# Kernel tuning notes

Measured on AMD Instinct MI355X. Metric: run time of the kernel, lower is better.

Reference implementation:

```python
import jax, jax.numpy as jnp
import numpy as np

N = 50000       # nodes
E = 800000      # edges (avg degree 16)
IN_F = 128
OUT_F = 128
NEG_SLOPE = 0.2  # LeakyReLU alpha
EPS = 1e-10


def setup_inputs() -> dict:
    key = jax.random.key(0)
    k1, k2, k3, k4 = jax.random.split(key, 4)
    h = jax.random.normal(k1, (N, IN_F), dtype=jnp.float32)
    edge_index = jax.random.randint(k2, (2, E), 0, N, dtype=jnp.int32)
    # nn.Linear(in, out, bias=False): weight is [out, in], Wh = h @ W.T
    W = jax.random.normal(k3, (OUT_F, IN_F), dtype=jnp.float32) * (1.0 / np.sqrt(IN_F))
    # a: [2*out, 1], xavier_uniform with gain=1.414
    lim = 1.414 * np.sqrt(6.0 / (2 * OUT_F + 1))
    a = jax.random.uniform(k4, (2 * OUT_F, 1), dtype=jnp.float32, minval=-lim, maxval=lim)
    return {"h": h, "edge_index": edge_index, "W": W, "a": a}


def reference(h, edge_index, W, a):
    Wh = h @ W.T                              # [N, out]
    rows = edge_index[0]
    cols = edge_index[1]
    # cat([Wh_i, Wh_j],1) @ a  ==  (Wh @ a1)[rows] + (Wh @ a2)[cols]
    a1 = a[:OUT_F, 0]
    a2 = a[OUT_F:, 0]
    s1 = Wh @ a1                              # [N]
    s2 = Wh @ a2                              # [N]
    e = jax.nn.leaky_relu(s1[rows] + s2[cols], negative_slope=NEG_SLOPE)  # [E]
    e = e - jnp.max(e)
    exp_e = jnp.exp(e)
    sum_exp = jax.ops.segment_sum(exp_e, rows, num_segments=N)            # [N]
    alpha = exp_e / (sum_exp[rows] + EPS)                                 # [E]
    # sparse.mm(adj_att, Wh): h_prime[i] = sum_j alpha_ij * Wh[j]
    h_prime = jax.ops.segment_sum(alpha[:, None] * Wh[cols], rows, num_segments=N)
    return jax.nn.elu(h_prime)
```

## Files before the change

### kernel.cpp

```cpp
#include <hip/hip_runtime.h>

constexpr int FD = 128;
constexpr int NBMAX = 512;
constexpr int CH1 = 4096;
constexpr int CAPB = 3072;

typedef __attribute__((ext_vector_type(8))) short short8;
typedef __attribute__((ext_vector_type(4))) float floatx4;

__device__ __forceinline__ unsigned fenc(float f) {
    unsigned u = __float_as_uint(f);
    return (u & 0x80000000u) ? ~u : (u | 0x80000000u);
}
__device__ __forceinline__ float fdec(unsigned e) {
    return (e & 0x80000000u) ? __uint_as_float(e & 0x7fffffffu)
                             : __uint_as_float(~e);
}

__device__ __forceinline__ unsigned bpack(float x, float y) {
    unsigned ux = __float_as_uint(x); ux += 0x7FFFu + ((ux >> 16) & 1u);
    unsigned uy = __float_as_uint(y); uy += 0x7FFFu + ((uy >> 16) & 1u);
    return (ux >> 16) | (uy & 0xFFFF0000u);
}

__global__ __launch_bounds__(128) void initwt_kernel(const float* __restrict__ W,
                                                     unsigned* __restrict__ Wb,
                                                     int* __restrict__ bcursor,
                                                     unsigned* __restrict__ maxslot) {
    int j = blockIdx.x, k = threadIdx.x;
    float w = W[(size_t)j * FD + k];
    float pw = __shfl_xor(w, 1, 64);
    if ((k & 1) == 0) Wb[(size_t)j * 64 + (k >> 1)] = bpack(w, pw);
    if (j == 0) {
        for (int i = k; i < NBMAX; i += 128) bcursor[i] = 0;
        if (k < 2) maxslot[k] = 0x007FFFFFu;
    }
}

union GBShared {
    struct {
        int cnt[NBMAX];
        int ex[NBMAX];
        int gbase[NBMAX];
        int wtot[8];
        unsigned stage[CH1];
    } bin;
    struct {
        float m1[8];
        float m2[8];
    } gm;
};

__global__ __launch_bounds__(512) void gembin_kernel(const float* __restrict__ h,
                                                     const unsigned* __restrict__ Wb,
                                                     const float* __restrict__ a,
                                                     const int* __restrict__ ei,
                                                     int* __restrict__ bcursor,
                                                     unsigned* __restrict__ Whb,
                                                     float* __restrict__ s1,
                                                     float* __restrict__ s2,
                                                     unsigned* __restrict__ ebuf,
                                                     unsigned* __restrict__ maxslot,
                                                     int n, int e_cnt, int ngemm) {
    __shared__ GBShared sh;
    int t = threadIdx.x;

    if ((int)blockIdx.x < ngemm) {
        int w = t >> 6, lane = t & 63;
        int quad = lane >> 4, c = lane & 15;
        int rbase = blockIdx.x * 128 + w * 16;
        int node = rbase + c;

        int arow = min(node, n - 1);
        const floatx4* hrow = (const floatx4*)(h + (size_t)arow * FD);
        union { uint4 u; short8 s; } hf[4];
#pragma unroll
        for (int kk = 0; kk < 4; ++kk) {
            int k0 = kk * 32 + quad * 8;
            floatx4 f0 = __builtin_nontemporal_load(hrow + (k0 >> 2));
            floatx4 f1 = __builtin_nontemporal_load(hrow + (k0 >> 2) + 1);
            hf[kk].u.x = bpack(f0.x, f0.y);
            hf[kk].u.y = bpack(f0.z, f0.w);
            hf[kk].u.z = bpack(f1.x, f1.y);
            hf[kk].u.w = bpack(f1.z, f1.w);
        }

        float p1 = 0.f, p2 = 0.f;

#pragma unroll
        for (int tt = 0; tt < 8; ++tt) {
            const uint4* wrow = (const uint4*)(Wb + (size_t)(tt * 16 + c) * 64 + quad * 4);
            union { uint4 u; short8 s; } wf0, wf1, wf2, wf3;
            wf0.u = wrow[0];
            wf1.u = wrow[4];
            wf2.u = wrow[8];
            wf3.u = wrow[12];
            floatx4 z = {0.f, 0.f, 0.f, 0.f};
            floatx4 c0 = __builtin_amdgcn_mfma_f32_16x16x32_bf16(wf0.s, hf[0].s, z, 0, 0, 0);
            floatx4 c1 = __builtin_amdgcn_mfma_f32_16x16x32_bf16(wf1.s, hf[1].s, z, 0, 0, 0);
            floatx4 c2 = __builtin_amdgcn_mfma_f32_16x16x32_bf16(wf2.s, hf[2].s, z, 0, 0, 0);
            floatx4 c3 = __builtin_amdgcn_mfma_f32_16x16x32_bf16(wf3.s, hf[3].s, z, 0, 0, 0);
            floatx4 acc = (c0 + c1) + (c2 + c3);
            float4 a1q = *(const float4*)(a + tt * 16 + quad * 4);
            float4 a2q = *(const float4*)(a + FD + tt * 16 + quad * 4);
            p1 = fmaf(acc.x, a1q.x, p1); p1 = fmaf(acc.y, a1q.y, p1);
            p1 = fmaf(acc.z, a1q.z, p1); p1 = fmaf(acc.w, a1q.w, p1);
            p2 = fmaf(acc.x, a2q.x, p2); p2 = fmaf(acc.y, a2q.y, p2);
            p2 = fmaf(acc.z, a2q.z, p2); p2 = fmaf(acc.w, a2q.w, p2);
            if (node < n) {
                uint2 pk2;
                pk2.x = bpack(acc.x, acc.y);
                pk2.y = bpack(acc.z, acc.w);
                *(uint2*)(Whb + (size_t)node * 64 + tt * 8 + quad * 2) = pk2;
            }
        }

        p1 += __shfl_xor(p1, 16, 64); p1 += __shfl_xor(p1, 32, 64);
        p2 += __shfl_xor(p2, 16, 64); p2 += __shfl_xor(p2, 32, 64);
        if (quad == 0 && node < n) { s1[node] = p1; s2[node] = p2; }

        float m1 = (node < n) ? p1 : -3.0e38f;
        float m2 = (node < n) ? p2 : -3.0e38f;
#pragma unroll
        for (int d = 1; d < 16; d <<= 1) {
            m1 = fmaxf(m1, __shfl_xor(m1, d, 64));
            m2 = fmaxf(m2, __shfl_xor(m2, d, 64));
        }
        if (lane == 0) { sh.gm.m1[w] = m1; sh.gm.m2[w] = m2; }
        __syncthreads();
        if (t == 0) {
            float g1 = -3.0e38f, g2 = -3.0e38f;
#pragma unroll
            for (int k = 0; k < 8; ++k) {
                g1 = fmaxf(g1, sh.gm.m1[k]);
                g2 = fmaxf(g2, sh.gm.m2[k]);
            }
            atomicMax(&maxslot[0], fenc(g1));
            atomicMax(&maxslot[1], fenc(g2));
        }
    } else {
        int bb = blockIdx.x - ngemm;
        sh.bin.cnt[t] = 0;
        __syncthreads();
        int base = bb * CH1;
        int m = min(CH1, e_cnt - base);

        unsigned pack[8];
        int rank[8], bkt[8];
        int nk = 0;
#pragma unroll
        for (int k = 0; k < 8; ++k) {
            int idx = t + k * 512;
            if (idx < m) {
                int ed = base + idx;
                int r  = __builtin_nontemporal_load(ei + ed);
                int cc = __builtin_nontemporal_load(ei + e_cnt + ed);
                unsigned p = ((unsigned)r << 16) | (unsigned)cc;
                int b = r >> 7;
                pack[k] = p;
                bkt[k] = b;
                rank[k] = atomicAdd(&sh.bin.cnt[b], 1);
                nk = k + 1;
            }
        }
        __syncthreads();

        int l = t & 63, w = t >> 6;
        int v = sh.bin.cnt[t];
        int iv = v;
#pragma unroll
        for (int d = 1; d < 64; d <<= 1) {
            int u = __shfl_up(iv, d, 64);
            if (l >= d) iv += u;
        }
        if (l == 63) sh.bin.wtot[w] = iv;
        __syncthreads();
        if (t == 0) {
            int s = 0;
#pragma unroll
            for (int k = 0; k < 8; ++k) { int x = sh.bin.wtot[k]; sh.bin.wtot[k] = s; s += x; }
        }
        __syncthreads();
        int excl = iv - v + sh.bin.wtot[w];
        sh.bin.ex[t] = excl;
        if (v > 0) sh.bin.gbase[t] = atomicAdd(&bcursor[t], v);
        __syncthreads();
#pragma unroll
        for (int k = 0; k < 8; ++k)
            if (k < nk) sh.bin.stage[sh.bin.ex[bkt[k]] + rank[k]] = pack[k];
        __syncthreads();
        for (int s = t; s < m; s += 512) {
            unsigned p = sh.bin.stage[s];
            int b = p >> 23;
            int pos = sh.bin.gbase[b] + (s - sh.bin.ex[b]);
            if (pos < CAPB) ebuf[(size_t)b * CAPB + pos] = p;
        }
    }
}

#define FMA8(bv, av)                                                    \
    acc[0] = fmaf(av, __uint_as_float((bv).x << 16), acc[0]);           \
    acc[1] = fmaf(av, __uint_as_float((bv).x & 0xFFFF0000u), acc[1]);   \
    acc[2] = fmaf(av, __uint_as_float((bv).y << 16), acc[2]);           \
    acc[3] = fmaf(av, __uint_as_float((bv).y & 0xFFFF0000u), acc[3]);   \
    acc[4] = fmaf(av, __uint_as_float((bv).z << 16), acc[4]);           \
    acc[5] = fmaf(av, __uint_as_float((bv).z & 0xFFFF0000u), acc[5]);   \
    acc[6] = fmaf(av, __uint_as_float((bv).w << 16), acc[6]);           \
    acc[7] = fmaf(av, __uint_as_float((bv).w & 0xFFFF0000u), acc[7]);

__global__ __launch_bounds__(1024) void agg_kernel(const unsigned* __restrict__ ebuf,
                                                   const int* __restrict__ bcnt,
                                                   const float* __restrict__ s1,
                                                   const float* __restrict__ s2,
                                                   const unsigned* __restrict__ Whb,
                                                   const unsigned* __restrict__ maxslot,
                                                   float* __restrict__ out, int n) {
    __shared__ uint2 pairs[CAPB];
    __shared__ int cnt[128];
    __shared__ int exs[128];
    __shared__ float invs[128];
    __shared__ float s1l[128];
    int b = blockIdx.x;
    int t = threadIdx.x;
    int row0 = b << 7;
    int m = min(bcnt[b], CAPB);

    if (t < 128) {
        cnt[t] = 0;
        int gr = row0 + t;
        s1l[t] = (gr < n) ? s1[gr] : 0.f;
    }
    __syncthreads();

    unsigned pk[3];
    int rk[3], lrr[3];
    float s2v[3];
    int nk = 0;
#pragma unroll
    for (int k = 0; k < 3; ++k) {
        int idx = t + (k << 10);
        if (idx < m) {
            unsigned p = ebuf[(size_t)b * CAPB + idx];
            int lr = (p >> 16) & 127;
            pk[nk] = p;
            lrr[nk] = lr;
            s2v[nk] = s2[p & 0xFFFFu];
            rk[nk] = atomicAdd(&cnt[lr], 1);
            ++nk;
        }
    }
    __syncthreads();

    if (t < 64) {
        int va = cnt[t], vb = cnt[t + 64];
        int ia = va, ib = vb;
#pragma unroll
        for (int d = 1; d < 64; d <<= 1) {
            int ua = __shfl_up(ia, d, 64);
            int ub = __shfl_up(ib, d, 64);
            if (t >= d) { ia += ua; ib += ub; }
        }
        int tot = __shfl(ia, 63, 64);
        exs[t] = ia - va;
        exs[t + 64] = tot + ib - vb;
    }
    __syncthreads();

    float M = fdec(maxslot[0]) + fdec(maxslot[1]);
    M = (M >= 0.f) ? M : 0.2f * M;

    for (int k = 0; k < nk; ++k) {
        unsigned p = pk[k];
        float sv = s1l[lrr[k]] + s2v[k];
        float le = (sv >= 0.f) ? sv : 0.2f * sv;
        float ev = __expf(le - M);
        pairs[exs[lrr[k]] + rk[k]] = make_uint2(p & 0xFFFFu, __float_as_uint(ev));
    }
    __syncthreads();

    {
        int hw = t >> 5, fl = t & 31;
        for (int r = hw; r < 128; r += 32) {
            int s0 = exs[r], d = cnt[r];
            float s = 0.f;
            for (int k2 = fl; k2 < d; k2 += 32)
                s += __uint_as_float(pairs[s0 + k2].y);
#pragma unroll
            for (int dd = 1; dd < 32; dd <<= 1)
                s += __shfl_xor(s, dd, 64);
            if (fl == 0) invs[r] = 1.0f / (s + 1e-10f);
        }
    }
    __syncthreads();

    int w = t >> 6, l = t & 63, q = l >> 4, fl2 = l & 15;
    for (int ni = (w << 3); ni < (w << 3) + 8; ++ni) {
        int node = row0 + ni;
        if (node >= n) break;
        int s0 = exs[ni], deg = cnt[ni];
        float acc[8] = {0.f, 0.f, 0.f, 0.f, 0.f, 0.f, 0.f, 0.f};
        int j = q;
        for (; j + 4 < deg; j += 8) {
            uint2 e0 = pairs[s0 + j];
            uint2 e1 = pairs[s0 + j + 4];
            uint4 b0 = *(const uint4*)(Whb + (size_t)e0.x * 64 + 4 * fl2);
            uint4 b1 = *(const uint4*)(Whb + (size_t)e1.x * 64 + 4 * fl2);
            float a0 = __uint_as_float(e0.y);
            float a1 = __uint_as_float(e1.y);
            FMA8(b0, a0)
            FMA8(b1, a1)
        }
        if (j < deg) {
            uint2 e0 = pairs[s0 + j];
            uint4 b0 = *(const uint4*)(Whb + (size_t)e0.x * 64 + 4 * fl2);
            float a0 = __uint_as_float(e0.y);
            FMA8(b0, a0)
        }
#pragma unroll
        for (int i = 0; i < 8; ++i) {
            acc[i] += __shfl_xor(acc[i], 16, 64);
            acc[i] += __shfl_xor(acc[i], 32, 64);
        }
        if (q < 2) {
            float inv = invs[ni];
            float v0 = (q ? acc[4] : acc[0]) * inv;
            float v1 = (q ? acc[5] : acc[1]) * inv;
            float v2 = (q ? acc[6] : acc[2]) * inv;
            float v3 = (q ? acc[7] : acc[3]) * inv;
            floatx4 r;
            r.x = (v0 > 0.f) ? v0 : expm1f(v0);
            r.y = (v1 > 0.f) ? v1 : expm1f(v1);
            r.z = (v2 > 0.f) ? v2 : expm1f(v2);
            r.w = (v3 > 0.f) ? v3 : expm1f(v3);
            __builtin_nontemporal_store(r, (floatx4*)(out + (size_t)node * FD + fl2 * 8 + q * 4));
        }
    }
}

extern "C" void kernel_launch(void* const* d_in, const int* in_sizes, int n_in,
                              void* d_out, int out_size, void* d_ws, size_t ws_size,
                              hipStream_t stream) {
    const float* h = (const float*)d_in[0];
    const int* ei  = (const int*)d_in[1];
    const float* W = (const float*)d_in[2];
    const float* a = (const float*)d_in[3];
    float* out = (float*)d_out;
    int n = in_sizes[0] / FD;
    int e = in_sizes[1] / 2;
    int nb = (n + 127) >> 7;

    char* ws = (char*)d_ws;
    size_t off = 0;
    auto alloc = [&](size_t bytes) -> void* {
        void* p = ws + off;
        off += bytes;
        off = (off + 255) & ~(size_t)255;
        return p;
    };
    unsigned* Whb     = (unsigned*)alloc((size_t)n * 64 * sizeof(unsigned));
    unsigned* Wb      = (unsigned*)alloc((size_t)FD * 64 * sizeof(unsigned));
    float*    s1      = (float*)alloc((size_t)n * sizeof(float));
    float*    s2      = (float*)alloc((size_t)n * sizeof(float));
    int*      bcursor = (int*)alloc((size_t)NBMAX * sizeof(int));
    unsigned* ebuf    = (unsigned*)alloc((size_t)NBMAX * CAPB * sizeof(unsigned));
    unsigned* maxslot = (unsigned*)alloc(2 * sizeof(unsigned));

    int ngemm = (n + 127) / 128;
    int nbin  = (e + CH1 - 1) / CH1;

    initwt_kernel<<<FD, 128, 0, stream>>>(W, Wb, bcursor, maxslot);
    gembin_kernel<<<ngemm + nbin, 512, 0, stream>>>(h, Wb, a, ei, bcursor, Whb,
                                                    s1, s2, ebuf, maxslot, n, e, ngemm);
    agg_kernel<<<nb, 1024, 0, stream>>>(ebuf, bcursor, s1, s2, Whb, maxslot, out, n);
}
```

Baseline: 145.4 us.

## Shrink aggregation buckets to 32 rows and use atomic softmax sums

Edges are now binned into buckets of 32 destination rows instead of 128, so the aggregation kernel launches about four times as many 256-thread blocks, each with a smaller shared staging buffer. This targets the poor load balance and occupancy of a few hundred 1024-thread blocks spread over the GPU. The binning scan now handles four buckets per thread and reuses the count array for offsets. The per-row exp-sum pass is replaced by shared-memory atomicAdd, and the gather loop is unrolled to four edges per step. The risks are the smaller per-bucket capacity (768), which could overflow for skewed degree distributions, and more global atomics on the bucket cursors.

```diff
diff --git a/kernel.cpp b/kernel.cpp
--- a/kernel.cpp
+++ b/kernel.cpp
@@ -1,9 +1,11 @@
 #include <hip/hip_runtime.h>
 
 constexpr int FD = 128;
-constexpr int NBMAX = 512;
+constexpr int BSH = 5;
+constexpr int BROWS = 32;
+constexpr int NBMAX = 2048;
 constexpr int CH1 = 4096;
-constexpr int CAPB = 3072;
+constexpr int CAPB = 768;
 
 typedef __attribute__((ext_vector_type(8))) short short8;
 typedef __attribute__((ext_vector_type(4))) float floatx4;
@@ -40,7 +42,6 @@
 union GBShared {
     struct {
         int cnt[NBMAX];
-        int ex[NBMAX];
         int gbase[NBMAX];
         int wtot[8];
         unsigned stage[CH1];
@@ -140,7 +141,8 @@
         }
     } else {
         int bb = blockIdx.x - ngemm;
-        sh.bin.cnt[t] = 0;
+#pragma unroll
+        for (int k = 0; k < 4; ++k) sh.bin.cnt[t + k * 512] = 0;
         __syncthreads();
         int base = bb * CH1;
         int m = min(CH1, e_cnt - base);
@@ -156,7 +158,7 @@
                 int r  = __builtin_nontemporal_load(ei + ed);
                 int cc = __builtin_nontemporal_load(ei + e_cnt + ed);
                 unsigned p = ((unsigned)r << 16) | (unsigned)cc;
-                int b = r >> 7;
+                int b = r >> BSH;
                 pack[k] = p;
                 bkt[k] = b;
                 rank[k] = atomicAdd(&sh.bin.cnt[b], 1);
@@ -166,8 +168,11 @@
         __syncthreads();
 
         int l = t & 63, w = t >> 6;
-        int v = sh.bin.cnt[t];
-        int iv = v;
+        int b4 = t * 4;
+        int v0 = sh.bin.cnt[b4], v1 = sh.bin.cnt[b4 + 1];
+        int v2 = sh.bin.cnt[b4 + 2], v3 = sh.bin.cnt[b4 + 3];
+        int lsum = v0 + v1 + v2 + v3;
+        int iv = lsum;
 #pragma unroll
         for (int d = 1; d < 64; d <<= 1) {
             int u = __shfl_up(iv, d, 64);
@@ -181,18 +186,24 @@
             for (int k = 0; k < 8; ++k) { int x = sh.bin.wtot[k]; sh.bin.wtot[k] = s; s += x; }
         }
         __syncthreads();
-        int excl = iv - v + sh.bin.wtot[w];
-        sh.bin.ex[t] = excl;
-        if (v > 0) sh.bin.gbase[t] = atomicAdd(&bcursor[t], v);
+        int off0 = iv - lsum + sh.bin.wtot[w];
+        sh.bin.cnt[b4]     = off0;
+        sh.bin.cnt[b4 + 1] = off0 + v0;
+        sh.bin.cnt[b4 + 2] = off0 + v0 + v1;
+        sh.bin.cnt[b4 + 3] = off0 + v0 + v1 + v2;
+        if (v0 > 0) sh.bin.gbase[b4]     = atomicAdd(&bcursor[b4], v0);
+        if (v1 > 0) sh.bin.gbase[b4 + 1] = atomicAdd(&bcursor[b4 + 1], v1);
+        if (v2 > 0) sh.bin.gbase[b4 + 2] = atomicAdd(&bcursor[b4 + 2], v2);
+        if (v3 > 0) sh.bin.gbase[b4 + 3] = atomicAdd(&bcursor[b4 + 3], v3);
         __syncthreads();
 #pragma unroll
         for (int k = 0; k < 8; ++k)
-            if (k < nk) sh.bin.stage[sh.bin.ex[bkt[k]] + rank[k]] = pack[k];
+            if (k < nk) sh.bin.stage[sh.bin.cnt[bkt[k]] + rank[k]] = pack[k];
         __syncthreads();
         for (int s = t; s < m; s += 512) {
             unsigned p = sh.bin.stage[s];
-            int b = p >> 23;
-            int pos = sh.bin.gbase[b] + (s - sh.bin.ex[b]);
+            int b = p >> (16 + BSH);
+            int pos = sh.bin.gbase[b] + (s - sh.bin.cnt[b]);
             if (pos < CAPB) ebuf[(size_t)b * CAPB + pos] = p;
         }
     }
@@ -208,25 +219,27 @@
     acc[6] = fmaf(av, __uint_as_float((bv).w << 16), acc[6]);           \
     acc[7] = fmaf(av, __uint_as_float((bv).w & 0xFFFF0000u), acc[7]);
 
-__global__ __launch_bounds__(1024) void agg_kernel(const unsigned* __restrict__ ebuf,
-                                                   const int* __restrict__ bcnt,
-                                                   const float* __restrict__ s1,
-                                                   const float* __restrict__ s2,
-                                                   const unsigned* __restrict__ Whb,
-                                                   const unsigned* __restrict__ maxslot,
-                                                   float* __restrict__ out, int n) {
+__global__ __launch_bounds__(256) void agg_kernel(const unsigned* __restrict__ ebuf,
+                                                  const int* __restrict__ bcnt,
+                                                  const float* __restrict__ s1,
+                                                  const float* __restrict__ s2,
+                                                  const unsigned* __restrict__ Whb,
+                                                  const unsigned* __restrict__ maxslot,
+                                                  float* __restrict__ out, int n) {
     __shared__ uint2 pairs[CAPB];
-    __shared__ int cnt[128];
-    __shared__ int exs[128];
-    __shared__ float invs[128];
-    __shared__ float s1l[128];
+    __shared__ int cnt[BROWS];
+    __shared__ int exs[BROWS];
+    __shared__ float sums[BROWS];
+    __shared__ float invs[BROWS];
+    __shared__ float s1l[BROWS];
     int b = blockIdx.x;
     int t = threadIdx.x;
-    int row0 = b << 7;
+    int row0 = b << BSH;
     int m = min(bcnt[b], CAPB);
 
-    if (t < 128) {
+    if (t < BROWS) {
         cnt[t] = 0;
+        sums[t] = 0.f;
         int gr = row0 + t;
         s1l[t] = (gr < n) ? s1[gr] : 0.f;
     }
@@ -238,10 +251,10 @@
     int nk = 0;
 #pragma unroll
     for (int k = 0; k < 3; ++k) {
-        int idx = t + (k << 10);
+        int idx = t + (k << 8);
         if (idx < m) {
-            unsigned p = ebuf[(size_t)b * CAPB + idx];
-            int lr = (p >> 16) & 127;
+            unsigned p = __builtin_nontemporal_load(ebuf + (size_t)b * CAPB + idx);
+            int lr = (p >> 16) & (BROWS - 1);
             pk[nk] = p;
             lrr[nk] = lr;
             s2v[nk] = s2[p & 0xFFFFu];
@@ -251,18 +264,15 @@
     }
     __syncthreads();
 
-    if (t < 64) {
-        int va = cnt[t], vb = cnt[t + 64];
-        int ia = va, ib = vb;
-#pragma unroll
-        for (int d = 1; d < 64; d <<= 1) {
-            int ua = __shfl_up(ia, d, 64);
-            int ub = __shfl_up(ib, d, 64);
-            if (t >= d) { ia += ua; ib += ub; }
-        }
-        int tot = __shfl(ia, 63, 64);
-        exs[t] = ia - va;
-        exs[t + 64] = tot + ib - vb;
+    if (t < BROWS) {
+        int v = cnt[t];
+        int iv = v;
+#pragma unroll
+        for (int d = 1; d < BROWS; d <<= 1) {
+            int u = __shfl_up(iv, d, 64);
+            if (t >= d) iv += u;
+        }
+        exs[t] = iv - v;
     }
     __syncthreads();
 
@@ -275,22 +285,10 @@
         float le = (sv >= 0.f) ? sv : 0.2f * sv;
         float ev = __expf(le - M);
         pairs[exs[lrr[k]] + rk[k]] = make_uint2(p & 0xFFFFu, __float_as_uint(ev));
-    }
-    __syncthreads();
-
-    {
-        int hw = t >> 5, fl = t & 31;
-        for (int r = hw; r < 128; r += 32) {
-            int s0 = exs[r], d = cnt[r];
-            float s = 0.f;
-            for (int k2 = fl; k2 < d; k2 += 32)
-                s += __uint_as_float(pairs[s0 + k2].y);
-#pragma unroll
-            for (int dd = 1; dd < 32; dd <<= 1)
-                s += __shfl_xor(s, dd, 64);
-            if (fl == 0) invs[r] = 1.0f / (s + 1e-10f);
-        }
-    }
+        atomicAdd(&sums[lrr[k]], ev);
+    }
+    __syncthreads();
+    if (t < BROWS) invs[t] = 1.0f / (sums[t] + 1e-10f);
     __syncthreads();
 
     int w = t >> 6, l = t & 63, q = l >> 4, fl2 = l & 15;
@@ -300,17 +298,25 @@
         int s0 = exs[ni], deg = cnt[ni];
         float acc[8] = {0.f, 0.f, 0.f, 0.f, 0.f, 0.f, 0.f, 0.f};
         int j = q;
-        for (; j + 4 < deg; j += 8) {
+        for (; j + 12 < deg; j += 16) {
             uint2 e0 = pairs[s0 + j];
             uint2 e1 = pairs[s0 + j + 4];
+            uint2 e2 = pairs[s0 + j + 8];
+            uint2 e3 = pairs[s0 + j + 12];
             uint4 b0 = *(const uint4*)(Whb + (size_t)e0.x * 64 + 4 * fl2);
             uint4 b1 = *(const uint4*)(Whb + (size_t)e1.x * 64 + 4 * fl2);
+            uint4 b2 = *(const uint4*)(Whb + (size_t)e2.x * 64 + 4 * fl2);
+            uint4 b3 = *(const uint4*)(Whb + (size_t)e3.x * 64 + 4 * fl2);
             float a0 = __uint_as_float(e0.y);
             float a1 = __uint_as_float(e1.y);
+            float a2 = __uint_as_float(e2.y);
+            float a3 = __uint_as_float(e3.y);
             FMA8(b0, a0)
             FMA8(b1, a1)
-        }
-        if (j < deg) {
+            FMA8(b2, a2)
+            FMA8(b3, a3)
+        }
+        for (; j < deg; j += 4) {
             uint2 e0 = pairs[s0 + j];
             uint4 b0 = *(const uint4*)(Whb + (size_t)e0.x * 64 + 4 * fl2);
             float a0 = __uint_as_float(e0.y);
@@ -347,7 +353,7 @@
     float* out = (float*)d_out;
     int n = in_sizes[0] / FD;
     int e = in_sizes[1] / 2;
-    int nb = (n + 127) >> 7;
+    int nb = (n + BROWS - 1) >> BSH;
 
     char* ws = (char*)d_ws;
     size_t off = 0;
@@ -371,5 +377,5 @@
     initwt_kernel<<<FD, 128, 0, stream>>>(W, Wb, bcursor, maxslot);
     gembin_kernel<<<ngemm + nbin, 512, 0, stream>>>(h, Wb, a, ei, bcursor, Whb,
                                                     s1, s2, ebuf, maxslot, n, e, ngemm);
-    agg_kernel<<<nb, 1024, 0, stream>>>(ebuf, bcursor, s1, s2, Whb, maxslot, out, n);
-}
+    agg_kernel<<<nb, 256, 0, stream>>>(ebuf, bcursor, s1, s2, Whb, maxslot, out, n);
+}
```

New measurement: 150.7 us. 3.7% more time.
